# Kernel tuning notes

Measured on AMD Instinct MI355X. Metric: run time of the kernel, lower is better.

The kernel has to match this reference:

```python
import jax, jax.numpy as jnp
import numpy as np

DIM = 512
NUM_GROUPS = 32
HEADS = 16
HEAD_DIM = 32
EPS = 1e-6


def group_norm(x, w, b, num_groups=NUM_GROUPS, eps=EPS):
    # x: [B, C, H, W]
    B, C, H, W = x.shape
    xg = x.reshape(B, num_groups, -1)
    mean = xg.mean(axis=-1, keepdims=True)
    var = xg.var(axis=-1, keepdims=True)
    xg = (xg - mean) / jnp.sqrt(var + eps)
    x = xg.reshape(B, C, H, W)
    return x * w[None, :, None, None] + b[None, :, None, None]


def conv1x1(x, w, b):
    # x: [B, C, H, W], w: [O, C], b: [O]
    return jnp.einsum('bchw,oc->bohw', x, w) + b[None, :, None, None]


def setup_inputs() -> dict:
    key = jax.random.key(0)
    ks = jax.random.split(key, 12)
    s = 1.0 / np.sqrt(DIM)
    d = {
        'x': jax.random.normal(ks[0], (1, DIM, 64, 64), dtype=jnp.float32),
        'gn_w': jnp.ones((DIM,), dtype=jnp.float32),
        'gn_b': jnp.zeros((DIM,), dtype=jnp.float32),
        'wq': jax.random.normal(ks[1], (DIM, DIM), dtype=jnp.float32) * s,
        'bq': jax.random.normal(ks[2], (DIM,), dtype=jnp.float32) * 0.01,
        'wk': jax.random.normal(ks[3], (DIM, DIM), dtype=jnp.float32) * s,
        'bk': jax.random.normal(ks[4], (DIM,), dtype=jnp.float32) * 0.01,
        'wv': jax.random.normal(ks[5], (DIM, DIM), dtype=jnp.float32) * s,
        'bv': jax.random.normal(ks[6], (DIM,), dtype=jnp.float32) * 0.01,
        'wo': jax.random.normal(ks[7], (DIM, DIM), dtype=jnp.float32) * s,
        'bo': jax.random.normal(ks[8], (DIM,), dtype=jnp.float32) * 0.01,
    }
    return d


def reference(x, gn_w, gn_b, wq, bq, wk, bk, wv, bv, wo, bo):
    B, C, H, W = x.shape
    N = H * W
    scale = HEAD_DIM ** -0.5

    q_in = x
    qn = group_norm(x, gn_w, gn_b)
    # Faithful to source: v-branch applies norm_q to the already-normalized q.
    vn = group_norm(qn, gn_w, gn_b)

    q = conv1x1(qn, wq, bq)
    k = conv1x1(vn, wk, bk)
    v = conv1x1(vn, wv, bv)

    def to_tokens(t):
        # [B, C, H, W] -> [B, heads, N, head_dim]
        return t.reshape(B, HEADS, HEAD_DIM, N).transpose(0, 1, 3, 2)

    q, k, v = to_tokens(q), to_tokens(k), to_tokens(v)

    attn = jax.nn.softmax(jnp.einsum('bhnd,bhmd->bhnm', q, k) * scale, axis=-1)
    out = jnp.einsum('bhnm,bhmd->bhnd', attn, v)  # [B, heads, N, head_dim]
    out = out.transpose(0, 1, 3, 2).reshape(B, C, H, W)
    out = conv1x1(out, wo, bo)
    return (out + q_in) / jnp.sqrt(jnp.float32(2.0))
```

## Files before the change

### kernel.cpp

```cpp
#include <hip/hip_runtime.h>

#define NTOK 4096
#define CHAN 512
#define GSIZE 65536
#define RSQRT2 0.7071067811865476f
#define SCALEX 0.2550348837f
#define WB_OFF 32768
#define QT_OFF (WB_OFF + 2097152)
#define WS_NEEDED ((size_t)(QT_OFF + 4194304))

typedef unsigned short ushort_t;
typedef __attribute__((ext_vector_type(8))) short bf16x8;
typedef __attribute__((ext_vector_type(8))) _Float16 f16x8;
typedef __attribute__((ext_vector_type(4))) float f32x4;

__device__ __forceinline__ ushort_t f2b(float f) {
    unsigned u = __float_as_uint(f);
    unsigned r = (u + 0x7FFFu + ((u >> 16) & 1u)) >> 16;
    return (ushort_t)r;
}
__device__ __forceinline__ unsigned pack2r(float a, float b) {
    unsigned ua = __float_as_uint(a), ub = __float_as_uint(b);
    return ((ua + 0x8000u) >> 16) | ((ub + 0x8000u) & 0xFFFF0000u);
}
__device__ __forceinline__ unsigned packh2(float a, float b) {
    return __builtin_bit_cast(unsigned, __builtin_amdgcn_cvt_pkrtz(a, b));
}
__device__ __forceinline__ ushort_t f2h(float f) {
    return (ushort_t)(packh2(f, f) & 0xFFFFu);
}
__device__ __forceinline__ bf16x8 ldfrag(const ushort_t* p) {
    return __builtin_bit_cast(bf16x8, *(const uint4*)p);
}
__device__ __forceinline__ f16x8 ldfragh(const ushort_t* p) {
    return __builtin_bit_cast(f16x8, *(const uint4*)p);
}
__device__ __forceinline__ float exp2_raw(float x) {
#if __has_builtin(__builtin_amdgcn_exp2f)
    return __builtin_amdgcn_exp2f(x);
#else
    return __expf(x * 0.6931471805599453f);
#endif
}
__device__ __forceinline__ void ldg2lds16(const void* g, void* l) {
    __builtin_amdgcn_global_load_lds(
        (const __attribute__((address_space(1))) void*)g,
        (__attribute__((address_space(3))) void*)l, 16, 0, 0);
}

__global__ void diag_kernel(float* out, float v) {
    if (threadIdx.x == 0 && blockIdx.x == 0) out[0] = v;
}

__global__ __launch_bounds__(256) void gn_sums(const float* __restrict__ x,
                                               float* __restrict__ S,
                                               float* __restrict__ SS) {
    int c = blockIdx.x, t = threadIdx.x;
    const float4* p = (const float4*)(x + (size_t)c * 4096);
    float s = 0.f, ss = 0.f;
    #pragma unroll
    for (int i = 0; i < 4; i++) {
        float4 f = p[i * 256 + t];
        s += f.x + f.y + f.z + f.w;
        ss += f.x * f.x + f.y * f.y + f.z * f.z + f.w * f.w;
    }
    #pragma unroll
    for (int off = 32; off > 0; off >>= 1) {
        s += __shfl_xor(s, off);
        ss += __shfl_xor(ss, off);
    }
    __shared__ float as[4], bs[4];
    int w = t >> 6;
    if ((t & 63) == 0) { as[w] = s; bs[w] = ss; }
    __syncthreads();
    if (t == 0) {
        S[c] = as[0] + as[1] + as[2] + as[3];
        SS[c] = bs[0] + bs[1] + bs[2] + bs[3];
    }
}

__global__ __launch_bounds__(512) void gn_coef(const float* __restrict__ S,
                                               const float* __restrict__ SS,
                                               const float* __restrict__ gnw,
                                               const float* __restrict__ gnb,
                                               float* __restrict__ qa,
                                               float* __restrict__ qd,
                                               float* __restrict__ va,
                                               float* __restrict__ vd) {
    int c = threadIdx.x;
    float Sc = S[c], SSc = SS[c];
    float gs = Sc, gss = SSc;
    #pragma unroll
    for (int off = 1; off < 16; off <<= 1) {
        gs += __shfl_xor(gs, off);
        gss += __shfl_xor(gss, off);
    }
    float mu = gs * (1.f / GSIZE);
    float var = gss * (1.f / GSIZE) - mu * mu;
    float r1 = rsqrtf(var + 1e-6f);
    float wc = gnw[c], bc = gnb[c];
    float a1 = r1 * wc;
    float d1 = bc - mu * a1;
    qa[c] = a1; qd[c] = d1;
    float S2 = a1 * Sc + 4096.f * d1;
    float SS2 = a1 * a1 * SSc + 2.f * a1 * d1 * Sc + 4096.f * d1 * d1;
    float gs2 = S2, gss2 = SS2;
    #pragma unroll
    for (int off = 1; off < 16; off <<= 1) {
        gs2 += __shfl_xor(gs2, off);
        gss2 += __shfl_xor(gss2, off);
    }
    float mu2 = gs2 * (1.f / GSIZE);
    float var2 = gss2 * (1.f / GSIZE) - mu2 * mu2;
    float r2 = rsqrtf(var2 + 1e-6f);
    float a2 = r2 * wc;
    va[c] = a1 * a2;
    vd[c] = a2 * (d1 - mu2) + bc;
}

__global__ __launch_bounds__(256) void prep_all(const float* __restrict__ wq,
                                                const float* __restrict__ wk,
                                                const float* __restrict__ wv,
                                                const float* __restrict__ wo,
                                                const float* __restrict__ bq,
                                                const float* __restrict__ bk,
                                                const float* __restrict__ bv,
                                                const float* __restrict__ qa,
                                                const float* __restrict__ qd,
                                                const float* __restrict__ va,
                                                const float* __restrict__ vd,
                                                float* __restrict__ bqf,
                                                float* __restrict__ bkf,
                                                float* __restrict__ bvf,
                                                ushort_t* __restrict__ Wb) {
    int bx = blockIdx.x;
    if (bx < 384) {
        int row = bx * 4 + (threadIdx.x >> 6);
        int lane = threadIdx.x & 63;
        int m = row >> 9;
        int o = row & 511;
        const float* W = (m == 0) ? wq : (m == 1) ? wk : wv;
        const float* b = (m == 0) ? bq : (m == 1) ? bk : bv;
        const float* d = (m == 0) ? qd : vd;
        float* outp    = (m == 0) ? bqf : (m == 1) ? bkf : bvf;
        const float4* wr = (const float4*)(W + (size_t)o * 512) + lane * 2;
        const float4* dr = (const float4*)d + lane * 2;
        float4 a0 = wr[0], a1 = wr[1], d0 = dr[0], d1 = dr[1];
        float acc = a0.x * d0.x + a0.y * d0.y + a0.z * d0.z + a0.w * d0.w
                  + a1.x * d1.x + a1.y * d1.y + a1.z * d1.z + a1.w * d1.w;
        #pragma unroll
        for (int off = 32; off > 0; off >>= 1) acc += __shfl_xor(acc, off);
        if (lane == 0) outp[o] = b[o] + acc;
    } else {
        int idx = bx - 384;
        int y = idx >> 8;
        const float* src = (y == 0) ? wq : (y == 1) ? wk : (y == 2) ? wv : wo;
        int i = ((idx & 255) * 256 + threadIdx.x) * 4;
        float4 f = *(const float4*)(src + i);
        if (y < 3) {
            const float* aff = (y == 0) ? qa : va;
            float4 a = *(const float4*)(aff + (i & 511));
            f.x *= a.x; f.y *= a.y; f.z *= a.z; f.w *= a.w;
        }
        uint2 u;
        u.x = pack2r(f.x, f.y);
        u.y = pack2r(f.z, f.w);
        *(uint2*)(Wb + (size_t)y * 262144 + i) = u;
    }
}

__global__ __launch_bounds__(256) void qkv_mfma(const float* __restrict__ x,
                                                const ushort_t* __restrict__ Wb,
                                                const float* __restrict__ bqf,
                                                const float* __restrict__ bkf,
                                                const float* __restrict__ bvf,
                                                ushort_t* __restrict__ QT,
                                                ushort_t* __restrict__ KT,
                                                ushort_t* __restrict__ Vb) {
    __shared__ __align__(16) ushort_t Wl[128][72];
    __shared__ __align__(16) ushort_t Bn[64][72];
    __shared__ __align__(16) ushort_t Tl[64][136];
    int t = threadIdx.x;
    int nbase = blockIdx.x << 6;
    int y = blockIdx.y;
    int buf = y >> 2;
    int obase = (y & 3) << 7;
    const ushort_t* Wsrc = Wb + (size_t)buf * 262144;
    const float* bias = (buf == 0) ? bqf : (buf == 1) ? bkf : bvf;

    int w = t >> 6, lane = t & 63, q15 = lane & 15, quad = lane >> 4;
    f32x4 acc[2][4];
    #pragma unroll
    for (int i = 0; i < 2; i++)
        #pragma unroll
        for (int j = 0; j < 4; j++) acc[i][j] = (f32x4){0.f, 0.f, 0.f, 0.f};

    int tok = t & 63, c8 = t >> 6;
    for (int ck = 0; ck < 512; ck += 64) {
        __syncthreads();
        #pragma unroll
        for (int i = 0; i < 4; i++) {
            int idx = 4 * t + i;
            int row = idx >> 3, seg = idx & 7;
            *(uint4*)&Wl[row][seg * 8] =
                *(const uint4*)&Wsrc[(size_t)(obase + row) * 512 + ck + seg * 8];
        }
        {
            float v[16];
            #pragma unroll
            for (int i = 0; i < 16; i++)
                v[i] = x[(size_t)(ck + c8 * 16 + i) * NTOK + nbase + tok];
            uint4 u0, u1;
            u0.x = pack2r(v[0], v[1]);   u0.y = pack2r(v[2], v[3]);
            u0.z = pack2r(v[4], v[5]);   u0.w = pack2r(v[6], v[7]);
            u1.x = pack2r(v[8], v[9]);   u1.y = pack2r(v[10], v[11]);
            u1.z = pack2r(v[12], v[13]); u1.w = pack2r(v[14], v[15]);
            *(uint4*)&Bn[tok][c8 * 16] = u0;
            *(uint4*)&Bn[tok][c8 * 16 + 8] = u1;
        }
        __syncthreads();
        #pragma unroll
        for (int kk = 0; kk < 2; kk++) {
            bf16x8 af0 = ldfrag(&Wl[w * 32 + q15][kk * 32 + quad * 8]);
            bf16x8 af1 = ldfrag(&Wl[w * 32 + 16 + q15][kk * 32 + quad * 8]);
            #pragma unroll
            for (int n8 = 0; n8 < 4; n8++) {
                bf16x8 bfv = ldfrag(&Bn[n8 * 16 + q15][kk * 32 + quad * 8]);
                acc[0][n8] = __builtin_amdgcn_mfma_f32_16x16x32_bf16(af0, bfv, acc[0][n8], 0, 0, 0);
                acc[1][n8] = __builtin_amdgcn_mfma_f32_16x16x32_bf16(af1, bfv, acc[1][n8], 0, 0, 0);
            }
        }
    }

    if (buf == 2) {
        #pragma unroll
        for (int mi = 0; mi < 2; mi++)
            #pragma unroll
            for (int r = 0; r < 4; r++) {
                int o = obase + w * 32 + mi * 16 + quad * 4 + r;
                float bo = bias[o];
                #pragma unroll
                for (int n8 = 0; n8 < 4; n8++)
                    Vb[(size_t)o * NTOK + nbase + n8 * 16 + q15] = f2h(acc[mi][n8][r] + bo);
            }
        return;
    }

    ushort_t* dstT = (buf == 0) ? QT : KT;
    float qs = (buf == 0) ? SCALEX : 1.0f;
    __syncthreads();
    #pragma unroll
    for (int mi = 0; mi < 2; mi++)
        #pragma unroll
        for (int r = 0; r < 4; r++) {
            int mloc = w * 32 + mi * 16 + quad * 4 + r;
            float bo = bias[obase + mloc];
            #pragma unroll
            for (int n8 = 0; n8 < 4; n8++)
                Tl[n8 * 16 + q15][mloc] = f2b((acc[mi][n8][r] + bo) * qs);
        }
    __syncthreads();
    #pragma unroll
    for (int i = 0; i < 4; i++) {
        int idx = 4 * t + i;
        int row = idx >> 4, ch = idx & 15;
        uint4 u = *(const uint4*)&Tl[row][ch * 8];
        *(uint4*)&dstT[(size_t)(nbase + row) * 512 + obase + ch * 8] = u;
    }
}

__global__ __launch_bounds__(512, 4) void attn_v14(ushort_t* __restrict__ QT,
                                                   const ushort_t* __restrict__ KT,
                                                   const ushort_t* __restrict__ V) {
    __shared__ __align__(16) ushort_t KtF[2][8192];
    __shared__ __align__(16) ushort_t VtF[2][8192];
    int h = blockIdx.y;
    int t = threadIdx.x;
    int w = t >> 6, lane = t & 63, q15 = lane & 15, quad = lane >> 4;
    int qbase = (blockIdx.x << 7) + w * 16;
    int hc = h * 32;
    const ushort_t* Vh = V + (size_t)hc * NTOK;

    bf16x8 qf = ldfrag(&QT[(size_t)(qbase + q15) * 512 + hc + quad * 8]);

    const uint4 onesu = {0x3C003C00u, 0x3C003C00u, 0x3C003C00u, 0x3C003C00u};
    const f16x8 ones = __builtin_bit_cast(f16x8, onesu);

    f32x4 o[2] = {{0.f, 0.f, 0.f, 0.f}, {0.f, 0.f, 0.f, 0.f}};
    f32x4 lacc = {0.f, 0.f, 0.f, 0.f};

    auto issue = [&](int j0, int b) {
        #pragma unroll
        for (int i = 0; i < 2; i++) {
            int sbase = (w << 6) + (i << 9);
            int idx = sbase + lane;
            int krow = idx >> 2;
            int gd = (idx & 3) ^ ((krow >> 1) & 3);
            int rp = krow & 63;
            int srcr = (krow & 192) | (rp & 0x23) | ((rp & 0x0C) << 1) | ((rp & 0x10) >> 2);
            ldg2lds16(&KT[(size_t)(j0 + srcr) * 512 + hc + gd * 8],
                      &KtF[b][sbase * 8]);
        }
        #pragma unroll
        for (int i = 0; i < 2; i++) {
            int sbase = (w << 6) + (i << 9);
            int idx = sbase + lane;
            int d = idx >> 5;
            int gd = (idx & 31) ^ (d & 7);
            ldg2lds16(&Vh[(size_t)d * NTOK + j0 + gd * 8],
                      &VtF[b][sbase * 8]);
        }
    };

    issue(0, 0);
    int ksp8 = (quad ^ ((q15 >> 1) & 3)) * 8;
    int vq = q15 & 7;

    for (int tt = 0; tt < 16; tt++) {
        int cur = tt & 1;
        __syncthreads();
        if (tt < 15) issue((tt + 1) << 8, cur ^ 1);
        const ushort_t* KtC = KtF[cur];
        const ushort_t* VtC = VtF[cur];

        #pragma unroll
        for (int h2 = 0; h2 < 4; h2++) {
            f32x4 st[4];
            __builtin_amdgcn_s_setprio(1);
            #pragma unroll
            for (int kt = 0; kt < 4; kt++) {
                bf16x8 kf = ldfrag(&KtC[(h2 * 64 + kt * 16 + q15) * 32 + ksp8]);
                f32x4 z = {0.f, 0.f, 0.f, 0.f};
                st[kt] = __builtin_amdgcn_mfma_f32_16x16x32_bf16(kf, qf, z, 0, 0, 0);
            }
            __builtin_amdgcn_s_setprio(0);

            #pragma unroll
            for (int kt = 0; kt < 4; kt++)
                #pragma unroll
                for (int r = 0; r < 4; r++)
                    st[kt][r] = exp2_raw(st[kt][r]);

            int g0 = ((h2 * 8 + quad) ^ vq) * 8;
            int g1 = g0 ^ 32;
            f16x8 v00 = ldfragh(&VtC[q15 * 256 + g0]);
            f16x8 v01 = ldfragh(&VtC[(16 + q15) * 256 + g0]);
            f16x8 v10 = ldfragh(&VtC[q15 * 256 + g1]);
            f16x8 v11 = ldfragh(&VtC[(16 + q15) * 256 + g1]);

            uint4 p0u, p1u;
            p0u.x = packh2(st[0][0], st[0][1]);
            p0u.y = packh2(st[0][2], st[0][3]);
            p0u.z = packh2(st[1][0], st[1][1]);
            p0u.w = packh2(st[1][2], st[1][3]);
            p1u.x = packh2(st[2][0], st[2][1]);
            p1u.y = packh2(st[2][2], st[2][3]);
            p1u.z = packh2(st[3][0], st[3][1]);
            p1u.w = packh2(st[3][2], st[3][3]);
            f16x8 pf0 = __builtin_bit_cast(f16x8, p0u);
            f16x8 pf1 = __builtin_bit_cast(f16x8, p1u);
            __builtin_amdgcn_s_setprio(1);
            o[0] = __builtin_amdgcn_mfma_f32_16x16x32_f16(pf0, v00, o[0], 0, 0, 0);
            o[1] = __builtin_amdgcn_mfma_f32_16x16x32_f16(pf0, v01, o[1], 0, 0, 0);
            lacc = __builtin_amdgcn_mfma_f32_16x16x32_f16(pf0, ones, lacc, 0, 0, 0);
            o[0] = __builtin_amdgcn_mfma_f32_16x16x32_f16(pf1, v10, o[0], 0, 0, 0);
            o[1] = __builtin_amdgcn_mfma_f32_16x16x32_f16(pf1, v11, o[1], 0, 0, 0);
            lacc = __builtin_amdgcn_mfma_f32_16x16x32_f16(pf1, ones, lacc, 0, 0, 0);
            __builtin_amdgcn_s_setprio(0);
        }
    }

    #pragma unroll
    for (int r = 0; r < 4; r++) {
        float li = 1.f / lacc[r];
        int q = quad * 4 + r;
        QT[(size_t)(qbase + q) * 512 + hc + q15]      = f2b(o[0][r] * li);
        QT[(size_t)(qbase + q) * 512 + hc + 16 + q15] = f2b(o[1][r] * li);
    }
}

__global__ __launch_bounds__(256) void oproj_mfma(const ushort_t* __restrict__ OT,
                                                  const ushort_t* __restrict__ Wob,
                                                  const float* __restrict__ bo,
                                                  const float* __restrict__ x,
                                                  float* __restrict__ out) {
    __shared__ __align__(16) ushort_t Wl[64][72];
    __shared__ __align__(16) ushort_t Bn[64][72];
    int t = threadIdx.x;
    int nbase = blockIdx.x << 6;
    int obase = blockIdx.y << 6;
    int w = t >> 6, lane = t & 63, q15 = lane & 15, quad = lane >> 4;

    f32x4 acc[4];
    #pragma unroll
    for (int i = 0; i < 4; i++) acc[i] = (f32x4){0.f, 0.f, 0.f, 0.f};

    for (int ck = 0; ck < 512; ck += 64) {
        __syncthreads();
        #pragma unroll
        for (int i = 0; i < 2; i++) {
            int idx = t * 2 + i;
            int row = idx >> 3, seg = idx & 7;
            *(uint4*)&Wl[row][seg * 8] =
                *(const uint4*)&Wob[(size_t)(obase + row) * 512 + ck + seg * 8];
            *(uint4*)&Bn[row][seg * 8] =
                *(const uint4*)&OT[(size_t)(nbase + row) * 512 + ck + seg * 8];
        }
        __syncthreads();
        #pragma unroll
        for (int kk = 0; kk < 2; kk++) {
            bf16x8 af = ldfrag(&Wl[w * 16 + q15][kk * 32 + quad * 8]);
            #pragma unroll
            for (int n8 = 0; n8 < 4; n8++) {
                bf16x8 bfv = ldfrag(&Bn[n8 * 16 + q15][kk * 32 + quad * 8]);
                acc[n8] = __builtin_amdgcn_mfma_f32_16x16x32_bf16(af, bfv, acc[n8], 0, 0, 0);
            }
        }
    }

    #pragma unroll
    for (int r = 0; r < 4; r++) {
        int o = obase + w * 16 + quad * 4 + r;
        float b = bo[o];
        #pragma unroll
        for (int n8 = 0; n8 < 4; n8++) {
            size_t idx = (size_t)o * NTOK + nbase + n8 * 16 + q15;
            out[idx] = (acc[n8][r] + b + x[idx]) * RSQRT2;
        }
    }
}

extern "C" void kernel_launch(void* const* d_in, const int* in_sizes, int n_in,
                              void* d_out, int out_size, void* d_ws, size_t ws_size,
                              hipStream_t stream) {
    const float* x   = (const float*)d_in[0];
    const float* gnw = (const float*)d_in[1];
    const float* gnb = (const float*)d_in[2];
    const float* wq  = (const float*)d_in[3];
    const float* bq  = (const float*)d_in[4];
    const float* wk  = (const float*)d_in[5];
    const float* bk  = (const float*)d_in[6];
    const float* wv  = (const float*)d_in[7];
    const float* bv  = (const float*)d_in[8];
    const float* wo  = (const float*)d_in[9];
    const float* bo  = (const float*)d_in[10];
    float* out = (float*)d_out;

    if (ws_size < WS_NEEDED) {
        diag_kernel<<<1, 64, 0, stream>>>(out, (float)(ws_size >> 16));
        return;
    }

    char* wsb = (char*)d_ws;
    float* S   = (float*)(wsb + 0);
    float* SS  = (float*)(wsb + 2048);
    float* qa  = (float*)(wsb + 4096);
    float* qd  = (float*)(wsb + 6144);
    float* va  = (float*)(wsb + 8192);
    float* vd  = (float*)(wsb + 10240);
    float* bqf = (float*)(wsb + 12288);
    float* bkf = (float*)(wsb + 14336);
    float* bvf = (float*)(wsb + 16384);
    ushort_t* Wb = (ushort_t*)(wsb + WB_OFF);
    ushort_t* QT = (ushort_t*)(wsb + QT_OFF);
    ushort_t* KT = (ushort_t*)d_out;
    ushort_t* Vb = (ushort_t*)d_out + (size_t)CHAN * NTOK;

    gn_sums<<<512, 256, 0, stream>>>(x, S, SS);
    gn_coef<<<1, 512, 0, stream>>>(S, SS, gnw, gnb, qa, qd, va, vd);
    prep_all<<<1408, 256, 0, stream>>>(wq, wk, wv, wo, bq, bk, bv,
                                       qa, qd, va, vd, bqf, bkf, bvf, Wb);

    qkv_mfma<<<dim3(64, 12), 256, 0, stream>>>(x, Wb, bqf, bkf, bvf, QT, KT, Vb);

    attn_v14<<<dim3(32, 16), 512, 0, stream>>>(QT, KT, Vb);

    oproj_mfma<<<dim3(64, 8), 256, 0, stream>>>(QT, Wb + (size_t)3 * 262144, bo, x, out);
}
```

Measured before the change: 163.1 us.

## Pre-transpose x to bf16 and double-buffer QKV GEMM loads via direct-to-LDS

Adds an xprep kernel that converts x to a token-major bf16 copy once. This removes the repeated strided fp32 loads and conversions that each of the 12 output-channel blocks did in the QKV GEMM. The QKV kernel now double-buffers its W and x tiles in a single shared buffer, fills them with asynchronous global-to-LDS loads, and uses an XOR-swizzled layout so the next tile loads while MFMAs run on the current one. The cost is an extra kernel launch, 4 MB more workspace traffic and a larger workspace requirement.

```diff
diff --git a/kernel.cpp b/kernel.cpp
--- a/kernel.cpp
+++ b/kernel.cpp
@@ -7,7 +7,8 @@
 #define SCALEX 0.2550348837f
 #define WB_OFF 32768
 #define QT_OFF (WB_OFF + 2097152)
-#define WS_NEEDED ((size_t)(QT_OFF + 4194304))
+#define XT_OFF (QT_OFF + 4194304)
+#define WS_NEEDED ((size_t)(XT_OFF + 4194304))
 
 typedef unsigned short ushort_t;
 typedef __attribute__((ext_vector_type(8))) short bf16x8;
@@ -169,7 +170,28 @@
     }
 }
 
-__global__ __launch_bounds__(256) void qkv_mfma(const float* __restrict__ x,
+__global__ __launch_bounds__(256) void xprep(const float* __restrict__ x,
+                                             ushort_t* __restrict__ xT) {
+    int bx = blockIdx.x;
+    int t0 = (bx & 63) << 6;
+    int c0 = (bx >> 6) << 6;
+    int t = threadIdx.x;
+    int tok = t & 63, c16 = t >> 6;
+    float v[16];
+    #pragma unroll
+    for (int i = 0; i < 16; i++)
+        v[i] = x[(size_t)(c0 + c16 * 16 + i) * NTOK + t0 + tok];
+    uint4 u0, u1;
+    u0.x = pack2r(v[0], v[1]);   u0.y = pack2r(v[2], v[3]);
+    u0.z = pack2r(v[4], v[5]);   u0.w = pack2r(v[6], v[7]);
+    u1.x = pack2r(v[8], v[9]);   u1.y = pack2r(v[10], v[11]);
+    u1.z = pack2r(v[12], v[13]); u1.w = pack2r(v[14], v[15]);
+    ushort_t* dst = xT + (size_t)(t0 + tok) * 512 + c0 + c16 * 16;
+    *(uint4*)dst = u0;
+    *(uint4*)(dst + 8) = u1;
+}
+
+__global__ __launch_bounds__(256) void qkv_mfma(const ushort_t* __restrict__ xT,
                                                 const ushort_t* __restrict__ Wb,
                                                 const float* __restrict__ bqf,
                                                 const float* __restrict__ bkf,
@@ -177,15 +199,13 @@
                                                 ushort_t* __restrict__ QT,
                                                 ushort_t* __restrict__ KT,
                                                 ushort_t* __restrict__ Vb) {
-    __shared__ __align__(16) ushort_t Wl[128][72];
-    __shared__ __align__(16) ushort_t Bn[64][72];
-    __shared__ __align__(16) ushort_t Tl[64][136];
+    __shared__ __align__(16) ushort_t SH[2][12288];
     int t = threadIdx.x;
     int nbase = blockIdx.x << 6;
     int y = blockIdx.y;
     int buf = y >> 2;
     int obase = (y & 3) << 7;
-    const ushort_t* Wsrc = Wb + (size_t)buf * 262144;
+    const ushort_t* Wsrc = Wb + (size_t)buf * 262144 + (size_t)obase * 512;
     const float* bias = (buf == 0) ? bqf : (buf == 1) ? bkf : bvf;
 
     int w = t >> 6, lane = t & 63, q15 = lane & 15, quad = lane >> 4;
@@ -195,37 +215,41 @@
         #pragma unroll
         for (int j = 0; j < 4; j++) acc[i][j] = (f32x4){0.f, 0.f, 0.f, 0.f};
 
-    int tok = t & 63, c8 = t >> 6;
-    for (int ck = 0; ck < 512; ck += 64) {
+    auto issue = [&](int ck, int b) {
+        ushort_t* base = SH[b];
+        #pragma unroll
+        for (int i = 0; i < 4; i++) {
+            int idx = t + (i << 8);
+            int row = idx >> 3, gs = idx & 7;
+            int g = gs ^ (row & 7);
+            ldg2lds16(&Wsrc[(size_t)row * 512 + ck + g * 8], &base[idx * 8]);
+        }
+        #pragma unroll
+        for (int i = 0; i < 2; i++) {
+            int idx = t + (i << 8);
+            int tok = idx >> 3, gs = idx & 7;
+            int g = gs ^ (tok & 7);
+            ldg2lds16(&xT[(size_t)(nbase + tok) * 512 + ck + g * 8],
+                      &base[8192 + idx * 8]);
+        }
+    };
+
+    issue(0, 0);
+    int swz = q15 & 7;
+    for (int s = 0; s < 8; s++) {
+        int cur = s & 1;
         __syncthreads();
-        #pragma unroll
-        for (int i = 0; i < 4; i++) {
-            int idx = 4 * t + i;
-            int row = idx >> 3, seg = idx & 7;
-            *(uint4*)&Wl[row][seg * 8] =
-                *(const uint4*)&Wsrc[(size_t)(obase + row) * 512 + ck + seg * 8];
-        }
-        {
-            float v[16];
-            #pragma unroll
-            for (int i = 0; i < 16; i++)
-                v[i] = x[(size_t)(ck + c8 * 16 + i) * NTOK + nbase + tok];
-            uint4 u0, u1;
-            u0.x = pack2r(v[0], v[1]);   u0.y = pack2r(v[2], v[3]);
-            u0.z = pack2r(v[4], v[5]);   u0.w = pack2r(v[6], v[7]);
-            u1.x = pack2r(v[8], v[9]);   u1.y = pack2r(v[10], v[11]);
-            u1.z = pack2r(v[12], v[13]); u1.w = pack2r(v[14], v[15]);
-            *(uint4*)&Bn[tok][c8 * 16] = u0;
-            *(uint4*)&Bn[tok][c8 * 16 + 8] = u1;
-        }
-        __syncthreads();
+        if (s < 7) issue((s + 1) * 64, cur ^ 1);
+        const ushort_t* Wl = SH[cur];
+        const ushort_t* Bn = SH[cur] + 8192;
         #pragma unroll
         for (int kk = 0; kk < 2; kk++) {
-            bf16x8 af0 = ldfrag(&Wl[w * 32 + q15][kk * 32 + quad * 8]);
-            bf16x8 af1 = ldfrag(&Wl[w * 32 + 16 + q15][kk * 32 + quad * 8]);
+            int g = (kk * 4 + quad) ^ swz;
+            bf16x8 af0 = ldfrag(&Wl[((w * 32 + q15) * 8 + g) * 8]);
+            bf16x8 af1 = ldfrag(&Wl[((w * 32 + 16 + q15) * 8 + g) * 8]);
             #pragma unroll
             for (int n8 = 0; n8 < 4; n8++) {
-                bf16x8 bfv = ldfrag(&Bn[n8 * 16 + q15][kk * 32 + quad * 8]);
+                bf16x8 bfv = ldfrag(&Bn[((n8 * 16 + q15) * 8 + g) * 8]);
                 acc[0][n8] = __builtin_amdgcn_mfma_f32_16x16x32_bf16(af0, bfv, acc[0][n8], 0, 0, 0);
                 acc[1][n8] = __builtin_amdgcn_mfma_f32_16x16x32_bf16(af1, bfv, acc[1][n8], 0, 0, 0);
             }
@@ -246,9 +270,9 @@
         return;
     }
 
-    ushort_t* dstT = (buf == 0) ? QT : KT;
+    ushort_t* Tl = SH[0];
+    __syncthreads();
     float qs = (buf == 0) ? SCALEX : 1.0f;
-    __syncthreads();
     #pragma unroll
     for (int mi = 0; mi < 2; mi++)
         #pragma unroll
@@ -257,14 +281,15 @@
             float bo = bias[obase + mloc];
             #pragma unroll
             for (int n8 = 0; n8 < 4; n8++)
-                Tl[n8 * 16 + q15][mloc] = f2b((acc[mi][n8][r] + bo) * qs);
+                Tl[(n8 * 16 + q15) * 136 + mloc] = f2b((acc[mi][n8][r] + bo) * qs);
         }
     __syncthreads();
+    ushort_t* dstT = (buf == 0) ? QT : KT;
     #pragma unroll
     for (int i = 0; i < 4; i++) {
         int idx = 4 * t + i;
         int row = idx >> 4, ch = idx & 15;
-        uint4 u = *(const uint4*)&Tl[row][ch * 8];
+        uint4 u = *(const uint4*)&Tl[row * 136 + ch * 8];
         *(uint4*)&dstT[(size_t)(nbase + row) * 512 + obase + ch * 8] = u;
     }
 }
@@ -463,6 +488,7 @@
     float* bvf = (float*)(wsb + 16384);
     ushort_t* Wb = (ushort_t*)(wsb + WB_OFF);
     ushort_t* QT = (ushort_t*)(wsb + QT_OFF);
+    ushort_t* xT = (ushort_t*)(wsb + XT_OFF);
     ushort_t* KT = (ushort_t*)d_out;
     ushort_t* Vb = (ushort_t*)d_out + (size_t)CHAN * NTOK;
 
@@ -470,8 +496,9 @@
     gn_coef<<<1, 512, 0, stream>>>(S, SS, gnw, gnb, qa, qd, va, vd);
     prep_all<<<1408, 256, 0, stream>>>(wq, wk, wv, wo, bq, bk, bv,
                                        qa, qd, va, vd, bqf, bkf, bvf, Wb);
-
-    qkv_mfma<<<dim3(64, 12), 256, 0, stream>>>(x, Wb, bqf, bkf, bvf, QT, KT, Vb);
+    xprep<<<512, 256, 0, stream>>>(x, xT);
+
+    qkv_mfma<<<dim3(64, 12), 256, 0, stream>>>(xT, Wb, bqf, bkf, bvf, QT, KT, Vb);
 
     attn_v14<<<dim3(32, 16), 512, 0, stream>>>(QT, KT, Vb);
 
```

After: 160.8 us. About the same (-1.4%).
